# Kernel tuning notes

Measured on AMD Instinct MI355X. Metric: run time of the kernel, lower is better.

Reference implementation:

```python
import jax, jax.numpy as jnp
import numpy as np

B, S, D = 4, 512, 256
NEG = -1e30  # finite stand-in for -inf so fully-masked row 0 stays NaN-free


def setup_inputs() -> dict:
    key = jax.random.key(0)
    ks = jax.random.split(key, 10)
    s = 0.02
    return {
        "x": jax.random.normal(ks[0], (B, S, D), dtype=jnp.float32),
        # edge_mlp: Linear(3D -> D), ReLU, Linear(D -> 1). Stored [in, out].
        "W1": jax.random.normal(ks[1], (3 * D, D), dtype=jnp.float32) * s,
        "b1": jnp.zeros((D,), dtype=jnp.float32),
        "w2": jax.random.normal(ks[2], (D, 1), dtype=jnp.float32) * s,
        "b2": jnp.zeros((1,), dtype=jnp.float32),
        "Wv": jax.random.normal(ks[3], (D, D), dtype=jnp.float32) * s,
        "bv": jnp.zeros((D,), dtype=jnp.float32),
        "Wo": jax.random.normal(ks[4], (D, D), dtype=jnp.float32) * s,
        "bo": jnp.zeros((D,), dtype=jnp.float32),
        "gamma": jnp.ones((D,), dtype=jnp.float32),
        "beta": jnp.zeros((D,), dtype=jnp.float32),
    }


def reference(x, W1, b1, w2, b2, Wv, bv, Wo, bo, gamma, beta):
    b, seq, d = x.shape
    # edge_mlp layer1 on concat([x_i, x_j, x_i - x_j]) decomposes linearly:
    # h[b,i,j,:] = x_i @ (Wa + Wc) + x_j @ (Wb - Wc) + b1
    Wa, Wb, Wc = W1[:d], W1[d:2 * d], W1[2 * d:]
    hi = jnp.einsum('bid,dh->bih', x, Wa + Wc)          # [B,S,D]
    hj = jnp.einsum('bjd,dh->bjh', x, Wb - Wc)          # [B,S,D]
    h = jax.nn.relu(hi[:, :, None, :] + hj[:, None, :, :] + b1)  # [B,S,S,D]
    scores = jnp.einsum('bijh,h->bij', h, w2[:, 0]) + b2[0]      # [B,S,S]
    # strictly-lower-triangular causal mask (j < i)
    mask = jnp.tril(jnp.ones((seq, seq), dtype=bool), k=-1)
    scores = jnp.where(mask, scores, NEG)
    attn = jax.nn.softmax(scores, axis=-1)
    # row i=0 has no valid edges (torch yields NaN there); zero it instead
    row_valid = mask.any(axis=-1)                       # [S]
    attn = attn * row_valid[None, :, None].astype(attn.dtype)
    values = jnp.einsum('bjd,de->bje', x, Wv) + bv      # [B,S,D]
    message = jnp.einsum('bij,bjd->bid', attn, values)  # [B,S,D]
    out = jnp.einsum('bid,de->bie', message, Wo) + bo
    out = x + out
    # LayerNorm over last dim, eps=1e-5, biased variance (torch default)
    mu = jnp.mean(out, axis=-1, keepdims=True)
    var = jnp.mean(jnp.square(out - mu), axis=-1, keepdims=True)
    out = (out - mu) * jax.lax.rsqrt(var + 1e-5) * gamma + beta
    return out
```

## Files before the change

kernel.cpp:

```cpp
#include <hip/hip_runtime.h>
#include <math.h>

#define D 256
#define S 512
#define M 2048
#define CH (64 * 1024)

typedef __attribute__((ext_vector_type(8))) short bf16x8;
typedef __attribute__((ext_vector_type(4))) float f32x4;
typedef _Float16 half2v __attribute__((ext_vector_type(2)));

__device__ inline ushort f2bf(float f) {
    union { float f; unsigned u; } v; v.f = f;
    unsigned r = v.u + 0x7FFFu + ((v.u >> 16) & 1u);
    return (ushort)(r >> 16);
}

__device__ inline ushort f2h(float f) {
    union { _Float16 h; ushort u; } v; v.h = (_Float16)f; return v.u;
}

__device__ inline uint pack2h(float a, float b) {
    union { half2v h; uint u; } v; v.h[0] = (_Float16)a; v.h[1] = (_Float16)b;
    return v.u;
}

__device__ inline uint addrelu2(uint a, uint b) {
    union { uint u; half2v h; } x, y;
    x.u = a; y.u = b;
    half2v s = x.h + y.h;
    half2v z = {};
    s = __builtin_elementwise_max(s, z);
    union { half2v h; uint u; } r; r.h = s; return r.u;
}

__device__ inline float fdot2u(uint a, uint b, float acc) {
    union { uint u; half2v h; } x, y;
    x.u = a; y.u = b;
    return __builtin_amdgcn_fdot2(x.h, y.h, acc, false);
}

__global__ __launch_bounds__(256) void qkv_pack_k(
    const float* __restrict__ x, const float* __restrict__ W1,
    const float* __restrict__ Wv, const float* __restrict__ Wo,
    const float* __restrict__ b1, const float* __restrict__ bv,
    ushort* __restrict__ hi, ushort* __restrict__ hj,
    ushort* __restrict__ vals_t, ushort* __restrict__ Wot)
{
    __shared__ union {
        ushort Bs[64][264];
        ushort lt[64][72];
    } sh;

    const int u = blockIdx.x;
    const int t = threadIdx.x;

    if (u >= 384) {
        const int unit = u - 384;
        const int a0 = (unit >> 2) * 64;
        const int b0 = (unit & 3) * 64;
        const int r = t >> 4;
        const int c = (t & 15) * 4;
#pragma unroll
        for (int p = 0; p < 4; ++p) {
            const int sr = b0 + p * 16 + r;
            float4 v = *(const float4*)(Wo + (size_t)sr * 256 + a0 + c);
            sh.lt[p * 16 + r][c + 0] = f2bf(v.x);
            sh.lt[p * 16 + r][c + 1] = f2bf(v.y);
            sh.lt[p * 16 + r][c + 2] = f2bf(v.z);
            sh.lt[p * 16 + r][c + 3] = f2bf(v.w);
        }
        __syncthreads();
#pragma unroll
        for (int p = 0; p < 4; ++p) {
            const int dr = p * 16 + r;
            ushort4 o = make_ushort4(sh.lt[c + 0][dr], sh.lt[c + 1][dr],
                                     sh.lt[c + 2][dr], sh.lt[c + 3][dr]);
            *(ushort4*)(Wot + (size_t)(a0 + dr) * 256 + b0 + c) = o;
        }
        return;
    }

    const int bn = u % 12, bm = u / 12;
    const int n0 = bn * 64, m0 = bm * 64;
    const int region = n0 >> 8, c0 = n0 & 255;

    {
        const int cl4 = (t & 15) * 4;
        const int kb = (t >> 4) * 16;
#pragma unroll
        for (int kk = 0; kk < 16; ++kk) {
            const int k = kb + kk;
            float4 v;
            if (region == 0) {
                float4 wa = *(const float4*)(W1 + (size_t)k * 256 + c0 + cl4);
                float4 wc = *(const float4*)(W1 + (size_t)(512 + k) * 256 + c0 + cl4);
                v = make_float4(wa.x + wc.x, wa.y + wc.y, wa.z + wc.z, wa.w + wc.w);
            } else if (region == 1) {
                float4 wb = *(const float4*)(W1 + (size_t)(256 + k) * 256 + c0 + cl4);
                float4 wc = *(const float4*)(W1 + (size_t)(512 + k) * 256 + c0 + cl4);
                v = make_float4(wb.x - wc.x, wb.y - wc.y, wb.z - wc.z, wb.w - wc.w);
            } else {
                v = *(const float4*)(Wv + (size_t)k * 256 + c0 + cl4);
            }
            sh.Bs[cl4 + 0][k] = f2bf(v.x);
            sh.Bs[cl4 + 1][k] = f2bf(v.y);
            sh.Bs[cl4 + 2][k] = f2bf(v.z);
            sh.Bs[cl4 + 3][k] = f2bf(v.w);
        }
    }
    __syncthreads();

    const int w = t >> 6, l = t & 63;
    const int q = l >> 4, ln = l & 15;
    const int wm = (w >> 1) * 32, wn = (w & 1) * 32;

    f32x4 acc[2][2] = {};
    for (int k0 = 0; k0 < 256; k0 += 32) {
        union { bf16x8 v; ushort s[8]; } a[2];
        bf16x8 b[2];
#pragma unroll
        for (int mt = 0; mt < 2; ++mt) {
            const float* xr = x + (size_t)(m0 + wm + mt * 16 + ln) * 256 + k0 + q * 8;
            float4 u0 = *(const float4*)xr;
            float4 u1 = *(const float4*)(xr + 4);
            a[mt].s[0] = f2bf(u0.x); a[mt].s[1] = f2bf(u0.y);
            a[mt].s[2] = f2bf(u0.z); a[mt].s[3] = f2bf(u0.w);
            a[mt].s[4] = f2bf(u1.x); a[mt].s[5] = f2bf(u1.y);
            a[mt].s[6] = f2bf(u1.z); a[mt].s[7] = f2bf(u1.w);
        }
#pragma unroll
        for (int nt = 0; nt < 2; ++nt)
            b[nt] = *(const bf16x8*)&sh.Bs[wn + nt * 16 + ln][k0 + q * 8];
#pragma unroll
        for (int mt = 0; mt < 2; ++mt)
#pragma unroll
            for (int nt = 0; nt < 2; ++nt)
                acc[mt][nt] = __builtin_amdgcn_mfma_f32_16x16x32_bf16(a[mt].v, b[nt], acc[mt][nt], 0, 0, 0);
    }

    if (region < 2) {
        ushort* dst = (region == 0) ? hi : hj;
#pragma unroll
        for (int nt = 0; nt < 2; ++nt) {
            const int col = c0 + wn + nt * 16 + ln;
            const float bias = (region == 0) ? b1[col] : 0.f;
#pragma unroll
            for (int mt = 0; mt < 2; ++mt)
#pragma unroll
                for (int r = 0; r < 4; ++r) {
                    const int row = m0 + wm + mt * 16 + q * 4 + r;
                    dst[(size_t)row * 256 + col] = f2h(acc[mt][nt][r] + bias);
                }
        }
    } else {
        __syncthreads();
#pragma unroll
        for (int nt = 0; nt < 2; ++nt) {
            const int cl = wn + nt * 16 + ln;
            const float bias = bv[c0 + cl];
#pragma unroll
            for (int mt = 0; mt < 2; ++mt)
#pragma unroll
                for (int r = 0; r < 4; ++r)
                    sh.lt[cl][wm + mt * 16 + q * 4 + r] = f2bf(acc[mt][nt][r] + bias);
        }
        __syncthreads();
        const int bb = m0 >> 9, jloc = m0 & 511;
#pragma unroll
        for (int p = 0; p < 2; ++p) {
            const int idx = p * 256 + t;
            const int e_l = idx & 63, jc = (idx >> 6) * 8;
            *(uint4*)(vals_t + ((size_t)(bb * 256 + c0 + e_l)) * 512 + jloc + jc) =
                *(const uint4*)&sh.lt[e_l][jc];
        }
    }
}

__global__ __launch_bounds__(256) void scores_k(
    const ushort* __restrict__ hi, const ushort* __restrict__ hj,
    const float* __restrict__ w2, float* __restrict__ sc)
{
    const int jt = blockIdx.x, it = blockIdx.y, bb = blockIdx.z;
    if (jt > 2 * it + 1) return;
    const int i0 = it * 64, j0 = jt * 32;
    const int t = threadIdx.x, w = t >> 6, l = t & 63;
    const int q = l >> 4, ln = l & 15;

    __shared__ __align__(16) uint His2u[16][64];
    __shared__ __align__(16) float Sst[64][36];
    __shared__ uint w2u[128];
    if (t < 64) {
        float4 wv = *(const float4*)(w2 + t * 4);
        w2u[t * 2 + 0] = pack2h(wv.x, wv.y);
        w2u[t * 2 + 1] = pack2h(wv.z, wv.w);
    }

    const int si = t & 63, sh_ = (t >> 6) * 8;
    const ushort* hisrc = hi + (size_t)((bb << 9) + i0 + si) * 256 + sh_;
    const int jrow = w * 8 + q * 2;
    const ushort* hj0 = hj + (size_t)((bb << 9) + j0 + jrow) * 256;
    const ushort* hj1 = hj0 + 256;

    float acc00 = 0.f, acc01 = 0.f, acc10 = 0.f, acc11 = 0.f;
    float acc20 = 0.f, acc21 = 0.f, acc30 = 0.f, acc31 = 0.f;

    for (int hc = 0; hc < 256; hc += 32) {
        uint4 a = *(const uint4*)(hisrc + hc);
        uint e0u[16], e1u[16];
#pragma unroll
        for (int c = 0; c < 4; ++c) {
            *(uint4*)&e0u[c * 4] = *(const uint4*)(hj0 + hc + c * 8);
            *(uint4*)&e1u[c * 4] = *(const uint4*)(hj1 + hc + c * 8);
        }
        __syncthreads();
        const int hp0 = sh_ >> 1;
        His2u[hp0 + 0][si] = a.x;
        His2u[hp0 + 1][si] = a.y;
        His2u[hp0 + 2][si] = a.z;
        His2u[hp0 + 3][si] = a.w;
        __syncthreads();
#pragma unroll
        for (int hp = 0; hp < 16; ++hp) {
            uint4 av = *(const uint4*)&His2u[hp][ln * 4];
            const uint wv = w2u[(hc >> 1) + hp];
            const uint f0 = e0u[hp], f1 = e1u[hp];
            acc00 = fdot2u(addrelu2(av.x, f0), wv, acc00);
            acc01 = fdot2u(addrelu2(av.x, f1), wv, acc01);
            acc10 = fdot2u(addrelu2(av.y, f0), wv, acc10);
            acc11 = fdot2u(addrelu2(av.y, f1), wv, acc11);
            acc20 = fdot2u(addrelu2(av.z, f0), wv, acc20);
            acc21 = fdot2u(addrelu2(av.z, f1), wv, acc21);
            acc30 = fdot2u(addrelu2(av.w, f0), wv, acc30);
            acc31 = fdot2u(addrelu2(av.w, f1), wv, acc31);
        }
    }

    Sst[ln * 4 + 0][jrow] = acc00;  Sst[ln * 4 + 0][jrow + 1] = acc01;
    Sst[ln * 4 + 1][jrow] = acc10;  Sst[ln * 4 + 1][jrow + 1] = acc11;
    Sst[ln * 4 + 2][jrow] = acc20;  Sst[ln * 4 + 2][jrow + 1] = acc21;
    Sst[ln * 4 + 3][jrow] = acc30;  Sst[ln * 4 + 3][jrow + 1] = acc31;
    __syncthreads();
    const int i_l = t >> 2, jc = (t & 3) * 8;
    float* dst = sc + ((size_t)bb << 18) + (size_t)(i0 + i_l) * 512 + j0 + jc;
    *(float4*)dst       = *(const float4*)&Sst[i_l][jc];
    *(float4*)(dst + 4) = *(const float4*)&Sst[i_l][jc + 4];
}

__global__ __launch_bounds__(512) void smpvout_k(
    const float* __restrict__ sc, const ushort* __restrict__ vals_t,
    const ushort* __restrict__ Wot, const float* __restrict__ x,
    const float* __restrict__ bo, const float* __restrict__ gamma,
    const float* __restrict__ beta, float* __restrict__ out)
{
    const int u = blockIdx.x;
    const int b = u >> 6, m0 = (u & 63) * 8;
    const int t = threadIdx.x, w = t >> 6, l = t & 63;
    const int q = l >> 4, ln = l & 15;

    __shared__ __align__(16) ushort attnS[16][520];
    __shared__ __align__(16) ushort msgS[16][264];
    __shared__ float redS[8][8], redQ[8][8];

    *(uint4*)&attnS[8 + (t >> 6)][(t & 63) * 8] = make_uint4(0, 0, 0, 0);

    {
        const int i = m0 + w;
        const float* srow = sc + ((size_t)b << 18) + (size_t)i * S;
        const int j0 = l * 8;
        float v[8];
        *(float4*)&v[0] = *(const float4*)(srow + j0);
        *(float4*)&v[4] = *(const float4*)(srow + j0 + 4);
        float mx = -3.0e38f;
#pragma unroll
        for (int k = 0; k < 8; ++k) {
            v[k] = (j0 + k < i) ? v[k] : -3.0e38f;
            mx = fmaxf(mx, v[k]);
        }
#pragma unroll
        for (int off = 32; off; off >>= 1) mx = fmaxf(mx, __shfl_xor(mx, off, 64));
        float e[8];
        float sum = 0.f;
#pragma unroll
        for (int k = 0; k < 8; ++k) {
            e[k] = __expf(v[k] - mx);
            sum += (j0 + k < i) ? e[k] : 0.f;
        }
#pragma unroll
        for (int off = 32; off; off >>= 1) sum += __shfl_xor(sum, off, 64);
        const float inv = (i > 0) ? (1.f / sum) : 0.f;
        ushort o[8];
#pragma unroll
        for (int k = 0; k < 8; ++k)
            o[k] = (j0 + k < i) ? f2bf(e[k] * inv) : (ushort)0;
        *(ushort4*)&attnS[w][j0]     = make_ushort4(o[0], o[1], o[2], o[3]);
        *(ushort4*)&attnS[w][j0 + 4] = make_ushort4(o[4], o[5], o[6], o[7]);
    }
    __syncthreads();

    const ushort* V = vals_t + (size_t)b * 256 * 512;
    f32x4 acc[2] = {};
    const int kmax = (m0 + 8 + 31) & ~31;
    for (int k0 = 0; k0 < kmax; k0 += 32) {
        bf16x8 a = *(const bf16x8*)&attnS[ln][k0 + q * 8];
#pragma unroll
        for (int nt = 0; nt < 2; ++nt) {
            bf16x8 bb = *(const bf16x8*)(V + (size_t)(w * 32 + nt * 16 + ln) * 512 + k0 + q * 8);
            acc[nt] = __builtin_amdgcn_mfma_f32_16x16x32_bf16(a, bb, acc[nt], 0, 0, 0);
        }
    }
#pragma unroll
    for (int nt = 0; nt < 2; ++nt)
#pragma unroll
        for (int r = 0; r < 4; ++r)
            msgS[q * 4 + r][w * 32 + nt * 16 + ln] = f2bf(acc[nt][r]);
    __syncthreads();

    f32x4 acc2[2] = {};
    for (int k0 = 0; k0 < 256; k0 += 32) {
        bf16x8 a = *(const bf16x8*)&msgS[ln][k0 + q * 8];
#pragma unroll
        for (int nt = 0; nt < 2; ++nt) {
            bf16x8 bb = *(const bf16x8*)(Wot + (size_t)(w * 32 + nt * 16 + ln) * 256 + k0 + q * 8);
            acc2[nt] = __builtin_amdgcn_mfma_f32_16x16x32_bf16(a, bb, acc2[nt], 0, 0, 0);
        }
    }

    const int r0 = (b << 9) + m0;
    float sum[4] = {}, sq[4] = {};
    if (q < 2) {
#pragma unroll
        for (int nt = 0; nt < 2; ++nt) {
            const int col = w * 32 + nt * 16 + ln;
            const float bov = bo[col];
#pragma unroll
            for (int r = 0; r < 4; ++r) {
                const int row = r0 + q * 4 + r;
                float v = acc2[nt][r] + x[(size_t)row * 256 + col] + bov;
                acc2[nt][r] = v;
                sum[r] += v;
                sq[r] += v * v;
            }
        }
    }
#pragma unroll
    for (int r = 0; r < 4; ++r) {
#pragma unroll
        for (int off = 1; off < 16; off <<= 1) {
            sum[r] += __shfl_xor(sum[r], off, 64);
            sq[r]  += __shfl_xor(sq[r],  off, 64);
        }
    }
    if (ln == 0 && q < 2) {
#pragma unroll
        for (int r = 0; r < 4; ++r) {
            redS[q * 4 + r][w] = sum[r];
            redQ[q * 4 + r][w] = sq[r];
        }
    }
    __syncthreads();
    if (q < 2) {
#pragma unroll
        for (int nt = 0; nt < 2; ++nt) {
            const int col = w * 32 + nt * 16 + ln;
            const float g = gamma[col], be = beta[col];
#pragma unroll
            for (int r = 0; r < 4; ++r) {
                const int rl = q * 4 + r;
                float ts = 0.f, tq = 0.f;
#pragma unroll
                for (int k = 0; k < 8; ++k) { ts += redS[rl][k]; tq += redQ[rl][k]; }
                const float mu = ts * (1.f / 256.f);
                const float var = tq * (1.f / 256.f) - mu * mu;
                out[(size_t)(r0 + rl) * 256 + col] =
                    (acc2[nt][r] - mu) * rsqrtf(var + 1e-5f) * g + be;
            }
        }
    }
}

extern "C" void kernel_launch(void* const* d_in, const int* in_sizes, int n_in,
                              void* d_out, int out_size, void* d_ws, size_t ws_size,
                              hipStream_t stream)
{
    (void)in_sizes; (void)n_in; (void)out_size; (void)ws_size;
    const float* x     = (const float*)d_in[0];
    const float* W1    = (const float*)d_in[1];
    const float* b1    = (const float*)d_in[2];
    const float* w2    = (const float*)d_in[3];
    const float* Wv    = (const float*)d_in[5];
    const float* bv    = (const float*)d_in[6];
    const float* Wo    = (const float*)d_in[7];
    const float* bo    = (const float*)d_in[8];
    const float* gamma = (const float*)d_in[9];
    const float* beta  = (const float*)d_in[10];
    float* out = (float*)d_out;

    float* ws = (float*)d_ws;
    ushort* hi     = (ushort*)ws;
    ushort* hj     = (ushort*)(ws + 8 * (size_t)CH);
    float*  sc     = ws + 16 * (size_t)CH;
    ushort* Wot    = (ushort*)(ws + 32 * (size_t)CH);
    ushort* vals_t = (ushort*)(ws + 33 * (size_t)CH);

    qkv_pack_k<<<dim3(400),      256, 0, stream>>>(x, W1, Wv, Wo, b1, bv, hi, hj, vals_t, Wot);
    scores_k  <<<dim3(16, 8, 4), 256, 0, stream>>>(hi, hj, w2, sc);
    smpvout_k <<<dim3(256),      512, 0, stream>>>(sc, vals_t, Wot, x, bo, gamma, beta, out);
}
```

Measured before the change: 126.4 us.

## Pre-pack hi in pair-interleaved layout, drop LDS staging, re-tile output kernel

The projection kernel now writes hi in a transposed layout that packs pairs of features, and writes hj through shared memory so the global stores are coalesced. With this layout the scores kernel reads hi straight from global memory and no longer needs the per-chunk shared-memory staging and its two barriers. The softmax/PV/output kernel moves to 4 rows per block with 256 threads, giving twice as many blocks, and each wave covers 64 columns. The trade-off is more global/L2 load traffic in the inner scores loop, and in the last kernel three quarters of the MFMA rows are padding.

```diff
diff --git a/kernel.cpp b/kernel.cpp
--- a/kernel.cpp
+++ b/kernel.cpp
@@ -5,6 +5,7 @@
 #define S 512
 #define M 2048
 #define CH (64 * 1024)
+#define LTW 76
 
 typedef __attribute__((ext_vector_type(8))) short bf16x8;
 typedef __attribute__((ext_vector_type(4))) float f32x4;
@@ -23,6 +24,10 @@
 __device__ inline uint pack2h(float a, float b) {
     union { half2v h; uint u; } v; v.h[0] = (_Float16)a; v.h[1] = (_Float16)b;
     return v.u;
+}
+
+__device__ inline uint pack2u(ushort a, ushort b) {
+    return (uint)a | ((uint)b << 16);
 }
 
 __device__ inline uint addrelu2(uint a, uint b) {
@@ -44,12 +49,12 @@
     const float* __restrict__ x, const float* __restrict__ W1,
     const float* __restrict__ Wv, const float* __restrict__ Wo,
     const float* __restrict__ b1, const float* __restrict__ bv,
-    ushort* __restrict__ hi, ushort* __restrict__ hj,
+    uint* __restrict__ hi_p, ushort* __restrict__ hj,
     ushort* __restrict__ vals_t, ushort* __restrict__ Wot)
 {
     __shared__ union {
         ushort Bs[64][264];
-        ushort lt[64][72];
+        ushort lt[64][LTW];
     } sh;
 
     const int u = blockIdx.x;
@@ -139,22 +144,54 @@
                 acc[mt][nt] = __builtin_amdgcn_mfma_f32_16x16x32_bf16(a[mt].v, b[nt], acc[mt][nt], 0, 0, 0);
     }
 
-    if (region < 2) {
-        ushort* dst = (region == 0) ? hi : hj;
+    __syncthreads();
+
+    if (region == 0) {
 #pragma unroll
         for (int nt = 0; nt < 2; ++nt) {
-            const int col = c0 + wn + nt * 16 + ln;
-            const float bias = (region == 0) ? b1[col] : 0.f;
+            const int cl = wn + nt * 16 + ln;
+            const float bias = b1[c0 + cl];
 #pragma unroll
             for (int mt = 0; mt < 2; ++mt)
 #pragma unroll
-                for (int r = 0; r < 4; ++r) {
-                    const int row = m0 + wm + mt * 16 + q * 4 + r;
-                    dst[(size_t)row * 256 + col] = f2h(acc[mt][nt][r] + bias);
-                }
+                for (int r = 0; r < 4; ++r)
+                    sh.lt[cl][wm + mt * 16 + q * 4 + r] = f2h(acc[mt][nt][r] + bias);
+        }
+        __syncthreads();
+#pragma unroll
+        for (int p = 0; p < 2; ++p) {
+            const int qid = p * 256 + t;
+            const int r4 = (qid & 15) * 4;
+            const int hpl = qid >> 4;
+            uint4 o;
+            o.x = pack2u(sh.lt[2 * hpl][r4 + 0], sh.lt[2 * hpl + 1][r4 + 0]);
+            o.y = pack2u(sh.lt[2 * hpl][r4 + 1], sh.lt[2 * hpl + 1][r4 + 1]);
+            o.z = pack2u(sh.lt[2 * hpl][r4 + 2], sh.lt[2 * hpl + 1][r4 + 2]);
+            o.w = pack2u(sh.lt[2 * hpl][r4 + 3], sh.lt[2 * hpl + 1][r4 + 3]);
+            *(uint4*)(hi_p + (size_t)((c0 >> 1) + hpl) * 2048 + m0 + r4) = o;
+        }
+    } else if (region == 1) {
+#pragma unroll
+        for (int nt = 0; nt < 2; ++nt) {
+            const int cl = wn + nt * 16 + ln;
+#pragma unroll
+            for (int mt = 0; mt < 2; ++mt)
+#pragma unroll
+                for (int r = 0; r < 4; ++r)
+                    sh.lt[cl][wm + mt * 16 + q * 4 + r] = f2h(acc[mt][nt][r]);
+        }
+        __syncthreads();
+#pragma unroll
+        for (int p = 0; p < 2; ++p) {
+            const int qid = p * 256 + t;
+            const int cg = qid & 7;
+            const int rl = qid >> 3;
+            ushort o[8];
+#pragma unroll
+            for (int k = 0; k < 8; ++k) o[k] = sh.lt[cg * 8 + k][rl];
+            *(uint4*)(hj + (size_t)(m0 + rl) * 256 + c0 + cg * 8) = *(const uint4*)o;
         }
     } else {
-        __syncthreads();
 #pragma unroll
         for (int nt = 0; nt < 2; ++nt) {
             const int cl = wn + nt * 16 + ln;
@@ -178,7 +215,7 @@
 }
 
 __global__ __launch_bounds__(256) void scores_k(
-    const ushort* __restrict__ hi, const ushort* __restrict__ hj,
+    const uint* __restrict__ hi_p, const ushort* __restrict__ hj,
     const float* __restrict__ w2, float* __restrict__ sc)
 {
     const int jt = blockIdx.x, it = blockIdx.y, bb = blockIdx.z;
@@ -187,7 +224,6 @@
     const int t = threadIdx.x, w = t >> 6, l = t & 63;
     const int q = l >> 4, ln = l & 15;
 
-    __shared__ __align__(16) uint His2u[16][64];
     __shared__ __align__(16) float Sst[64][36];
     __shared__ uint w2u[128];
     if (t < 64) {
@@ -195,9 +231,9 @@
         w2u[t * 2 + 0] = pack2h(wv.x, wv.y);
         w2u[t * 2 + 1] = pack2h(wv.z, wv.w);
     }
-
-    const int si = t & 63, sh_ = (t >> 6) * 8;
-    const ushort* hisrc = hi + (size_t)((bb << 9) + i0 + si) * 256 + sh_;
+    __syncthreads();
+
+    const size_t gi = (size_t)((bb << 9) + i0 + ln * 4);
     const int jrow = w * 8 + q * 2;
     const ushort* hj0 = hj + (size_t)((bb << 9) + j0 + jrow) * 256;
     const ushort* hj1 = hj0 + 256;
@@ -206,24 +242,17 @@
     float acc20 = 0.f, acc21 = 0.f, acc30 = 0.f, acc31 = 0.f;
 
     for (int hc = 0; hc < 256; hc += 32) {
-        uint4 a = *(const uint4*)(hisrc + hc);
+        const int hp0 = hc >> 1;
         uint e0u[16], e1u[16];
 #pragma unroll
         for (int c = 0; c < 4; ++c) {
             *(uint4*)&e0u[c * 4] = *(const uint4*)(hj0 + hc + c * 8);
             *(uint4*)&e1u[c * 4] = *(const uint4*)(hj1 + hc + c * 8);
         }
-        __syncthreads();
-        const int hp0 = sh_ >> 1;
-        His2u[hp0 + 0][si] = a.x;
-        His2u[hp0 + 1][si] = a.y;
-        His2u[hp0 + 2][si] = a.z;
-        His2u[hp0 + 3][si] = a.w;
-        __syncthreads();
 #pragma unroll
         for (int hp = 0; hp < 16; ++hp) {
-            uint4 av = *(const uint4*)&His2u[hp][ln * 4];
-            const uint wv = w2u[(hc >> 1) + hp];
+            uint4 av = *(const uint4*)(hi_p + (size_t)(hp0 + hp) * 2048 + gi);
+            const uint wv = w2u[hp0 + hp];
             const uint f0 = e0u[hp], f1 = e1u[hp];
             acc00 = fdot2u(addrelu2(av.x, f0), wv, acc00);
             acc01 = fdot2u(addrelu2(av.x, f1), wv, acc01);
@@ -247,22 +276,24 @@
     *(float4*)(dst + 4) = *(const float4*)&Sst[i_l][jc + 4];
 }
 
-__global__ __launch_bounds__(512) void smpvout_k(
+__global__ __launch_bounds__(256) void smpvout_k(
     const float* __restrict__ sc, const ushort* __restrict__ vals_t,
     const ushort* __restrict__ Wot, const float* __restrict__ x,
     const float* __restrict__ bo, const float* __restrict__ gamma,
     const float* __restrict__ beta, float* __restrict__ out)
 {
     const int u = blockIdx.x;
-    const int b = u >> 6, m0 = (u & 63) * 8;
+    const int b = u >> 7, m0 = (u & 127) * 4;
     const int t = threadIdx.x, w = t >> 6, l = t & 63;
     const int q = l >> 4, ln = l & 15;
 
     __shared__ __align__(16) ushort attnS[16][520];
     __shared__ __align__(16) ushort msgS[16][264];
-    __shared__ float redS[8][8], redQ[8][8];
-
-    *(uint4*)&attnS[8 + (t >> 6)][(t & 63) * 8] = make_uint4(0, 0, 0, 0);
+    __shared__ float redS[4][4], redQ[4][4];
+
+#pragma unroll
+    for (int p = 0; p < 3; ++p)
+        *(uint4*)&attnS[4 + w + p * 4][l * 8] = make_uint4(0, 0, 0, 0);
 
     {
         const int i = m0 + w;
@@ -299,43 +330,43 @@
     __syncthreads();
 
     const ushort* V = vals_t + (size_t)b * 256 * 512;
-    f32x4 acc[2] = {};
-    const int kmax = (m0 + 8 + 31) & ~31;
+    f32x4 acc[4] = {};
+    const int kmax = (m0 + 4 + 31) & ~31;
     for (int k0 = 0; k0 < kmax; k0 += 32) {
         bf16x8 a = *(const bf16x8*)&attnS[ln][k0 + q * 8];
 #pragma unroll
-        for (int nt = 0; nt < 2; ++nt) {
-            bf16x8 bb = *(const bf16x8*)(V + (size_t)(w * 32 + nt * 16 + ln) * 512 + k0 + q * 8);
+        for (int nt = 0; nt < 4; ++nt) {
+            bf16x8 bb = *(const bf16x8*)(V + (size_t)(w * 64 + nt * 16 + ln) * 512 + k0 + q * 8);
             acc[nt] = __builtin_amdgcn_mfma_f32_16x16x32_bf16(a, bb, acc[nt], 0, 0, 0);
         }
     }
 #pragma unroll
-    for (int nt = 0; nt < 2; ++nt)
+    for (int nt = 0; nt < 4; ++nt)
 #pragma unroll
         for (int r = 0; r < 4; ++r)
-            msgS[q * 4 + r][w * 32 + nt * 16 + ln] = f2bf(acc[nt][r]);
-    __syncthreads();
-
-    f32x4 acc2[2] = {};
+            msgS[q * 4 + r][w * 64 + nt * 16 + ln] = f2bf(acc[nt][r]);
+    __syncthreads();
+
+    f32x4 acc2[4] = {};
     for (int k0 = 0; k0 < 256; k0 += 32) {
         bf16x8 a = *(const bf16x8*)&msgS[ln][k0 + q * 8];
 #pragma unroll
-        for (int nt = 0; nt < 2; ++nt) {
-            bf16x8 bb = *(const bf16x8*)(Wot + (size_t)(w * 32 + nt * 16 + ln) * 256 + k0 + q * 8);
+        for (int nt = 0; nt < 4; ++nt) {
+            bf16x8 bb = *(const bf16x8*)(Wot + (size_t)(w * 64 + nt * 16 + ln) * 256 + k0 + q * 8);
             acc2[nt] = __builtin_amdgcn_mfma_f32_16x16x32_bf16(a, bb, acc2[nt], 0, 0, 0);
         }
     }
 
     const int r0 = (b << 9) + m0;
     float sum[4] = {}, sq[4] = {};
-    if (q < 2) {
-#pragma unroll
-        for (int nt = 0; nt < 2; ++nt) {
-            const int col = w * 32 + nt * 16 + ln;
+    if (q == 0) {
+#pragma unroll
+        for (int nt = 0; nt < 4; ++nt) {
+            const int col = w * 64 + nt * 16 + ln;
             const float bov = bo[col];
 #pragma unroll
             for (int r = 0; r < 4; ++r) {
-                const int row = r0 + q * 4 + r;
+                const int row = r0 + r;
                 float v = acc2[nt][r] + x[(size_t)row * 256 + col] + bov;
                 acc2[nt][r] = v;
                 sum[r] += v;
@@ -351,28 +382,26 @@
             sq[r]  += __shfl_xor(sq[r],  off, 64);
         }
     }
-    if (ln == 0 && q < 2) {
+    if (ln == 0 && q == 0) {
 #pragma unroll
         for (int r = 0; r < 4; ++r) {
-            redS[q * 4 + r][w] = sum[r];
-            redQ[q * 4 + r][w] = sq[r];
-        }
-    }
-    __syncthreads();
-    if (q < 2) {
-#pragma unroll
-        for (int nt = 0; nt < 2; ++nt) {
-            const int col = w * 32 + nt * 16 + ln;
+            redS[r][w] = sum[r];
+            redQ[r][w] = sq[r];
+        }
+    }
+    __syncthreads();
+    if (q == 0) {
+#pragma unroll
+        for (int nt = 0; nt < 4; ++nt) {
+            const int col = w * 64 + nt * 16 + ln;
             const float g = gamma[col], be = beta[col];
 #pragma unroll
             for (int r = 0; r < 4; ++r) {
-                const int rl = q * 4 + r;
-                float ts = 0.f, tq = 0.f;
-#pragma unroll
-                for (int k = 0; k < 8; ++k) { ts += redS[rl][k]; tq += redQ[rl][k]; }
+                const float ts = redS[r][0] + redS[r][1] + redS[r][2] + redS[r][3];
+                const float tq = redQ[r][0] + redQ[r][1] + redQ[r][2] + redQ[r][3];
                 const float mu = ts * (1.f / 256.f);
                 const float var = tq * (1.f / 256.f) - mu * mu;
-                out[(size_t)(r0 + rl) * 256 + col] =
+                out[(size_t)(r0 + r) * 256 + col] =
                     (acc2[nt][r] - mu) * rsqrtf(var + 1e-5f) * g + be;
             }
         }
@@ -397,13 +426,13 @@
     float* out = (float*)d_out;
 
     float* ws = (float*)d_ws;
-    ushort* hi     = (ushort*)ws;
-    ushort* hj     = (ushort*)(ws + 8 * (size_t)CH);
-    float*  sc     = ws + 16 * (size_t)CH;
-    ushort* Wot    = (ushort*)(ws + 32 * (size_t)CH);
-    ushort* vals_t = (ushort*)(ws + 33 * (size_t)CH);
-
-    qkv_pack_k<<<dim3(400),      256, 0, stream>>>(x, W1, Wv, Wo, b1, bv, hi, hj, vals_t, Wot);
-    scores_k  <<<dim3(16, 8, 4), 256, 0, stream>>>(hi, hj, w2, sc);
-    smpvout_k <<<dim3(256),      512, 0, stream>>>(sc, vals_t, Wot, x, bo, gamma, beta, out);
-}
+    uint*   hi_p   = (uint*)ws;
+    ushort* hj     = (ushort*)(ws + 4 * (size_t)CH);
+    float*  sc     = ws + 8 * (size_t)CH;
+    ushort* Wot    = (ushort*)(ws + 24 * (size_t)CH);
+    ushort* vals_t = (ushort*)(ws + 25 * (size_t)CH);
+
+    qkv_pack_k<<<dim3(400),      256, 0, stream>>>(x, W1, Wv, Wo, b1, bv, hi_p, hj, vals_t, Wot);
+    scores_k  <<<dim3(16, 8, 4), 256, 0, stream>>>(hi_p, hj, w2, sc);
+    smpvout_k <<<dim3(512),      256, 0, stream>>>(sc, vals_t, Wot, x, bo, gamma, beta, out);
+}
```

New measurement: 163.1 us. 29.0% more time.
